# Kernel optimization log

Measured on AMD Instinct MI355X. Metric: run time of the kernel, lower is better.

Reference implementation:

```python
import jax, jax.numpy as jnp
import numpy as np

KERNEL_SIZE = 5
EPS = 1e-6


def setup_inputs() -> dict:
    key = jax.random.key(0)
    k1, k2 = jax.random.split(key)
    b, c, h, w = 16, 512, 64, 64
    hidden = 512
    input_dim = c + KERNEL_SIZE * KERNEL_SIZE  # 537
    x = jax.random.normal(k1, (b, c, h, w), dtype=jnp.float32)
    # 1x1 conv weight, stored as (out, in); kaiming-ish scale
    W = jax.random.normal(k2, (hidden, input_dim), dtype=jnp.float32) * (1.0 / np.sqrt(input_dim))
    bias = jnp.zeros((hidden,), dtype=jnp.float32)
    return {"x": x, "W": W, "bias": bias}


def spatial_descriptor(x, k):
    # x: (b,c,h,w) -> (b, k*k, h, w), local self-similarity (dot product) volume
    b, c, h, w = x.shape
    p = k // 2
    xp = jnp.pad(x, ((0, 0), (0, 0), (p, p), (p, p)))
    # small fixed loop over k*k offsets; each term is a fused multiply-reduce
    corrs = [
        jnp.sum(x * jax.lax.dynamic_slice(xp, (0, 0, di, dj), (b, c, h, w)), axis=1)
        for di in range(k)
        for dj in range(k)
    ]
    return jnp.stack(corrs, axis=1)  # (b, k*k, h, w)


def reference(x, W, bias):
    k = KERNEL_SIZE
    gs = spatial_descriptor(x, k)  # (b, k^2, h, w)
    # featureL2Norm over channel dim (note: eps added to sum-of-squares, then sqrt)
    norm = jnp.sqrt(jnp.sum(gs * gs, axis=1, keepdims=True) + EPS)
    gs = gs / norm
    feat = jnp.concatenate([x, gs], axis=1)  # (b, c+k^2, h, w)
    # 1x1 conv + ReLU
    out = jnp.einsum('bchw,oc->bohw', feat, W) + bias[None, :, None, None]
    return jax.nn.relu(out)
```

## Files before the change

kernel.cpp:

```cpp
#include <hip/hip_runtime.h>
#include <stdint.h>

#define C_IN 512
#define HW 4096
#define NPIX 65536
#define KPAD 544
#define KIN 537
#define HID 512

typedef __attribute__((ext_vector_type(8))) short bf16x8;
typedef __attribute__((ext_vector_type(4))) float f32x4;

__device__ __forceinline__ unsigned short f2bf(float f) {
  union { float f; uint32_t u; } v; v.f = f;
  uint32_t u = v.u;
  return (unsigned short)((u + 0x7fffu + ((u >> 16) & 1u)) >> 16);
}
__device__ __forceinline__ float bf2f(unsigned short h) {
  union { uint32_t u; float f; } v; v.u = ((uint32_t)h) << 16;
  return v.f;
}

__global__ void k_wconv(const float* __restrict__ W, unsigned short* __restrict__ Wb) {
  int idx = blockIdx.x * 256 + threadIdx.x;
  if (idx >= HID * KPAD) return;
  int o = idx / KPAD;
  int k = idx - o * KPAD;
  float v = (k < KIN) ? W[o * KIN + k] : 0.f;
  Wb[idx] = f2bf(v);
}

__global__ __launch_bounds__(256, 8) void k_xpose(const float* __restrict__ x,
                                                  unsigned short* __restrict__ featB) {
  __shared__ unsigned short sm[64][70];
  int g = blockIdx.x;
  int b = g >> 9, cg = (g >> 6) & 7, pt = g & 63;
  int c0 = cg * 64, p0 = pt * 64;
  int t = threadIdx.x, lane = t & 63, w = t >> 6;
  const float* xb = x + ((size_t)b * C_IN + c0) * HW + p0;
#pragma unroll
  for (int i = 0; i < 8; ++i) {
    int ch = w * 16 + i * 2;
    float a = xb[(size_t)ch * HW + lane];
    float bq = xb[(size_t)(ch + 1) * HW + lane];
    uint32_t pk = (uint32_t)f2bf(a) | ((uint32_t)f2bf(bq) << 16);
    *(uint32_t*)&sm[lane][ch] = pk;
  }
  __syncthreads();
#pragma unroll
  for (int i = 0; i < 2; ++i) {
    int px = (t >> 3) + i * 32, kg = t & 7;
    int n = b * 4096 + p0 + px;
    *(bf16x8*)(featB + (size_t)n * KPAD + c0 + kg * 8) = *(const bf16x8*)&sm[px][kg * 8];
  }
}

__device__ __forceinline__ int xelem(int sr, int sc, int kg) {
  return (sr * 20 + sc) * 64 + ((kg ^ (sc & 7)) * 8);
}

__global__ __launch_bounds__(256, 8) void k_corr(const unsigned short* __restrict__ featB,
                                                 unsigned short* __restrict__ part) {
  __shared__ unsigned short xt[8 * 20 * 64];
  int g = blockIdx.x;
  int bid = (g & 7) * 1024 + (g >> 3);
  int cs = bid & 7;
  int cg = (bid >> 3) & 3;
  int rg = (bid >> 5) & 15;
  int b  = bid >> 9;
  int t = threadIdx.x;
  int lane = t & 63;
  int w = t >> 6;
  int r0 = rg * 4, c0 = cg * 16;

  bf16x8 v[5];
  int la[5];
#pragma unroll
  for (int i = 0; i < 5; ++i) {
    int flat = t + i * 256;
    int kg = flat & 7, pxi = flat >> 3;
    int sc = pxi % 20, sr = pxi / 20;
    int ir = r0 - 2 + sr, ic = c0 - 2 + sc;
    la[i] = xelem(sr, sc, kg);
    if ((unsigned)ir < 64u && (unsigned)ic < 64u) {
      int n = b * 4096 + ir * 64 + ic;
      v[i] = *(const bf16x8*)(featB + (size_t)n * KPAD + cs * 64 + kg * 8);
    } else {
      v[i] = (bf16x8){0, 0, 0, 0, 0, 0, 0, 0};
    }
  }
#pragma unroll
  for (int i = 0; i < 5; ++i)
    *(bf16x8*)&xt[la[i]] = v[i];
  __syncthreads();

  int i15 = lane & 15;
  int tq = lane >> 4;
  int q = i15 - tq * 4;
  bool valid = (q >= 0) && (q < 4);

  bf16x8 afr[2];
#pragma unroll
  for (int ks = 0; ks < 2; ++ks)
    afr[ks] = *(const bf16x8*)&xt[xelem(w + 2, 2 + i15, ks * 4 + tq)];

  int nb = b * 4096 + (r0 + w) * 64 + c0;
#pragma unroll 1
  for (int di = 0; di < 5; ++di) {
    int sr = w + di;
    unsigned short* pbase = part + ((size_t)(cs * 25 + di * 5)) * NPIX + nb;
#pragma unroll
    for (int dj = 0; dj < 5; ++dj) {
      f32x4 acc = (f32x4){0.f, 0.f, 0.f, 0.f};
#pragma unroll
      for (int ks = 0; ks < 2; ++ks) {
        bf16x8 bfr = *(const bf16x8*)&xt[xelem(sr, dj + i15, ks * 4 + tq)];
        acc = __builtin_amdgcn_mfma_f32_16x16x32_bf16(afr[ks], bfr, acc, 0, 0, 0);
      }
      float val = (q == 0) ? acc[0]
                : (q == 1) ? acc[1]
                : (q == 2) ? acc[2] : acc[3];
      if (valid) pbase[(size_t)dj * NPIX + i15] = f2bf(val);
    }
  }
}

__global__ void k_norm(const unsigned short* __restrict__ part,
                       unsigned short* __restrict__ featB) {
  int n = blockIdx.x * 256 + threadIdx.x;
  float g[25];
  float ss = 0.f;
#pragma unroll
  for (int k = 0; k < 25; ++k) {
    float s = 0.f;
#pragma unroll
    for (int cs = 0; cs < 8; ++cs)
      s += bf2f(part[((size_t)cs * 25 + k) * NPIX + n]);
    g[k] = s;
    ss += s * s;
  }
  float inv = 1.0f / sqrtf(ss + 1e-6f);
  unsigned short buf[32];
#pragma unroll
  for (int k = 0; k < 25; ++k) buf[k] = f2bf(g[k] * inv);
#pragma unroll
  for (int k = 25; k < 32; ++k) buf[k] = 0;
#pragma unroll
  for (int j = 0; j < 4; ++j)
    *(bf16x8*)(featB + (size_t)n * KPAD + 512 + j * 8) = *(bf16x8*)&buf[j * 8];
}

typedef __attribute__((address_space(3))) unsigned int as3_uint;
typedef const __attribute__((address_space(1))) unsigned int as1_uint;

__device__ __forceinline__ void glds16(const void* g, void* l) {
  __builtin_amdgcn_global_load_lds((as1_uint*)g, (as3_uint*)l, 16, 0, 0);
}

__global__ __launch_bounds__(256) void k_gemm(const unsigned short* __restrict__ Wb,
                                              const unsigned short* __restrict__ featB,
                                              const float* __restrict__ bias,
                                              float* __restrict__ out) {
  __shared__ __attribute__((aligned(16))) unsigned short As[2][4096];
  __shared__ __attribute__((aligned(16))) unsigned short Bs[2][4096];
  int g = blockIdx.x;
  int bid = (g & 7) * 256 + (g >> 3);
  int mt = bid & 3;
  int nt = bid >> 2;
  int m0 = mt * 128;
  int n0 = nt * 128;
  int tid = threadIdx.x;
  int wave = tid >> 6;
  int lane = tid & 63;
  int wm = wave >> 1;
  int wn = wave & 1;
  int kg = lane >> 4;

  uint32_t aOff[4], bOff[4];
#pragma unroll
  for (int r = 0; r < 4; ++r) {
    int rr = wm * 64 + r * 16 + (lane & 15);
    aOff[r] = rr * 64 + ((kg ^ ((rr >> 1) & 3)) << 4);
  }
#pragma unroll
  for (int cb = 0; cb < 4; ++cb) {
    int rr = wn * 64 + cb * 16 + (lane & 15);
    bOff[cb] = rr * 64 + ((kg ^ ((rr >> 1) & 3)) << 4);
  }

  f32x4 acc[4][4];
#pragma unroll
  for (int r = 0; r < 4; ++r)
#pragma unroll
    for (int cb = 0; cb < 4; ++cb)
      acc[r][cb] = (f32x4){0.f, 0.f, 0.f, 0.f};

  auto STAGE = [&](int buf, int k0) {
#pragma unroll
    for (int qq = 0; qq < 2; ++qq) {
      int ci = wave * 2 + qq;
      int i = ci * 64 + lane;
      int rr = i >> 2;
      int slot = i & 3;
      int k8 = slot ^ ((rr >> 1) & 3);
      glds16(Wb + (size_t)(m0 + rr) * KPAD + k0 + k8 * 8, (char*)&As[buf][0] + ci * 1024);
      glds16(featB + (size_t)(n0 + rr) * KPAD + k0 + k8 * 8, (char*)&Bs[buf][0] + ci * 1024);
    }
  };

  STAGE(0, 0);
  __syncthreads();
  int cur = 0;
#pragma unroll 1
  for (int t = 0; t < 17; ++t) {
    if (t < 16) STAGE(cur ^ 1, (t + 1) * 32);
    const char* Ab = (const char*)&As[cur][0];
    const char* Bb = (const char*)&Bs[cur][0];
    bf16x8 af[4], bf[4];
#pragma unroll
    for (int r = 0; r < 4; ++r)
      af[r] = *(const bf16x8*)(Ab + aOff[r]);
#pragma unroll
    for (int cb = 0; cb < 4; ++cb)
      bf[cb] = *(const bf16x8*)(Bb + bOff[cb]);
#pragma unroll
    for (int cb = 0; cb < 4; ++cb)
#pragma unroll
      for (int r = 0; r < 4; ++r)
        acc[r][cb] = __builtin_amdgcn_mfma_f32_16x16x32_bf16(af[r], bf[cb], acc[r][cb], 0, 0, 0);
    __syncthreads();
    cur ^= 1;
  }

  int bb = n0 >> 12;
  int hwb = n0 & 4095;
  float* outb = out + (size_t)bb * (HID * HW) + hwb;
#pragma unroll
  for (int r = 0; r < 4; ++r) {
    int row0 = m0 + wm * 64 + r * 16 + (lane >> 4) * 4;
    float bv[4];
#pragma unroll
    for (int j = 0; j < 4; ++j) bv[j] = bias[row0 + j];
#pragma unroll
    for (int cb = 0; cb < 4; ++cb) {
      int col = wn * 64 + cb * 16 + (lane & 15);
#pragma unroll
      for (int j = 0; j < 4; ++j) {
        float v2 = acc[r][cb][j] + bv[j];
        v2 = fmaxf(v2, 0.f);
        outb[(size_t)(row0 + j) * HW + col] = v2;
      }
    }
  }
}

extern "C" void kernel_launch(void* const* d_in, const int* in_sizes, int n_in,
                              void* d_out, int out_size, void* d_ws, size_t ws_size,
                              hipStream_t stream) {
  const float* x = (const float*)d_in[0];
  const float* W = (const float*)d_in[1];
  const float* bias = (const float*)d_in[2];
  float* out = (float*)d_out;
  char* ws = (char*)d_ws;
  unsigned short* featB = (unsigned short*)ws;
  unsigned short* Wb = (unsigned short*)(ws + 71303168);
  unsigned short* part = (unsigned short*)(ws + 71860224);

  k_wconv<<<1088, 256, 0, stream>>>(W, Wb);
  k_xpose<<<8192, 256, 0, stream>>>(x, featB);
  k_corr<<<8192, 256, 0, stream>>>(featB, part);
  k_norm<<<256, 256, 0, stream>>>(part, featB);
  k_gemm<<<2048, 256, 0, stream>>>(Wb, featB, bias, out);
}
```

Measured before the change: 151.2 us.

## Fuse channel-split correlation and L2 normalization into one kernel

The correlation kernel now loops over all 8 channel slices inside each block and accumulates the 25 offsets in registers. It normalizes and writes the descriptor directly into the feature buffer, so the bf16 partial-sum buffer and the separate norm kernel are removed. This cuts a kernel launch and the global round-trip of the partials, and keeps the per-slice sums in fp32 rather than rounding them to bf16. The trade-off is 8x fewer blocks (1024), each running a serial loop with syncs and 25 extra accumulator registers, so there is less parallelism for hiding latency. The same buffer is passed as both the read-only and the written pointer, but the two touch disjoint columns.

```diff
diff --git a/kernel.cpp b/kernel.cpp
--- a/kernel.cpp
+++ b/kernel.cpp
@@ -15,10 +15,6 @@
   union { float f; uint32_t u; } v; v.f = f;
   uint32_t u = v.u;
   return (unsigned short)((u + 0x7fffu + ((u >> 16) & 1u)) >> 16);
-}
-__device__ __forceinline__ float bf2f(unsigned short h) {
-  union { uint32_t u; float f; } v; v.u = ((uint32_t)h) << 16;
-  return v.f;
 }
 
 __global__ void k_wconv(const float* __restrict__ W, unsigned short* __restrict__ Wb) {
@@ -59,95 +55,91 @@
   return (sr * 20 + sc) * 64 + ((kg ^ (sc & 7)) * 8);
 }
 
-__global__ __launch_bounds__(256, 8) void k_corr(const unsigned short* __restrict__ featB,
-                                                 unsigned short* __restrict__ part) {
+__global__ __launch_bounds__(256, 4) void k_corr(const unsigned short* __restrict__ featRO,
+                                                 unsigned short* __restrict__ featB) {
   __shared__ unsigned short xt[8 * 20 * 64];
   int g = blockIdx.x;
-  int bid = (g & 7) * 1024 + (g >> 3);
-  int cs = bid & 7;
-  int cg = (bid >> 3) & 3;
-  int rg = (bid >> 5) & 15;
-  int b  = bid >> 9;
+  int bid = (g & 7) * 128 + (g >> 3);
+  int cg = bid & 3;
+  int rg = (bid >> 2) & 15;
+  int b  = bid >> 6;
   int t = threadIdx.x;
   int lane = t & 63;
   int w = t >> 6;
   int r0 = rg * 4, c0 = cg * 16;
-
-  bf16x8 v[5];
-  int la[5];
-#pragma unroll
-  for (int i = 0; i < 5; ++i) {
-    int flat = t + i * 256;
-    int kg = flat & 7, pxi = flat >> 3;
-    int sc = pxi % 20, sr = pxi / 20;
-    int ir = r0 - 2 + sr, ic = c0 - 2 + sc;
-    la[i] = xelem(sr, sc, kg);
-    if ((unsigned)ir < 64u && (unsigned)ic < 64u) {
-      int n = b * 4096 + ir * 64 + ic;
-      v[i] = *(const bf16x8*)(featB + (size_t)n * KPAD + cs * 64 + kg * 8);
-    } else {
-      v[i] = (bf16x8){0, 0, 0, 0, 0, 0, 0, 0};
-    }
-  }
-#pragma unroll
-  for (int i = 0; i < 5; ++i)
-    *(bf16x8*)&xt[la[i]] = v[i];
-  __syncthreads();
-
   int i15 = lane & 15;
   int tq = lane >> 4;
   int q = i15 - tq * 4;
-  bool valid = (q >= 0) && (q < 4);
-
-  bf16x8 afr[2];
-#pragma unroll
-  for (int ks = 0; ks < 2; ++ks)
-    afr[ks] = *(const bf16x8*)&xt[xelem(w + 2, 2 + i15, ks * 4 + tq)];
-
-  int nb = b * 4096 + (r0 + w) * 64 + c0;
+  bool valid = (i15 >> 2) == tq;
+
+  float acc_s[25];
+#pragma unroll
+  for (int k = 0; k < 25; ++k) acc_s[k] = 0.f;
+
 #pragma unroll 1
-  for (int di = 0; di < 5; ++di) {
-    int sr = w + di;
-    unsigned short* pbase = part + ((size_t)(cs * 25 + di * 5)) * NPIX + nb;
-#pragma unroll
-    for (int dj = 0; dj < 5; ++dj) {
-      f32x4 acc = (f32x4){0.f, 0.f, 0.f, 0.f};
-#pragma unroll
-      for (int ks = 0; ks < 2; ++ks) {
-        bf16x8 bfr = *(const bf16x8*)&xt[xelem(sr, dj + i15, ks * 4 + tq)];
-        acc = __builtin_amdgcn_mfma_f32_16x16x32_bf16(afr[ks], bfr, acc, 0, 0, 0);
+  for (int cs = 0; cs < 8; ++cs) {
+    bf16x8 v[5];
+    int la[5];
+#pragma unroll
+    for (int i = 0; i < 5; ++i) {
+      int flat = t + i * 256;
+      int kg = flat & 7, pxi = flat >> 3;
+      int sc = pxi % 20, sr = pxi / 20;
+      int ir = r0 - 2 + sr, ic = c0 - 2 + sc;
+      la[i] = xelem(sr, sc, kg);
+      if ((unsigned)ir < 64u && (unsigned)ic < 64u) {
+        int n = b * 4096 + ir * 64 + ic;
+        v[i] = *(const bf16x8*)(featRO + (size_t)n * KPAD + cs * 64 + kg * 8);
+      } else {
+        v[i] = (bf16x8){0, 0, 0, 0, 0, 0, 0, 0};
       }
-      float val = (q == 0) ? acc[0]
-                : (q == 1) ? acc[1]
-                : (q == 2) ? acc[2] : acc[3];
-      if (valid) pbase[(size_t)dj * NPIX + i15] = f2bf(val);
-    }
-  }
-}
-
-__global__ void k_norm(const unsigned short* __restrict__ part,
-                       unsigned short* __restrict__ featB) {
-  int n = blockIdx.x * 256 + threadIdx.x;
-  float g[25];
-  float ss = 0.f;
-#pragma unroll
-  for (int k = 0; k < 25; ++k) {
-    float s = 0.f;
-#pragma unroll
-    for (int cs = 0; cs < 8; ++cs)
-      s += bf2f(part[((size_t)cs * 25 + k) * NPIX + n]);
-    g[k] = s;
-    ss += s * s;
-  }
-  float inv = 1.0f / sqrtf(ss + 1e-6f);
-  unsigned short buf[32];
-#pragma unroll
-  for (int k = 0; k < 25; ++k) buf[k] = f2bf(g[k] * inv);
-#pragma unroll
-  for (int k = 25; k < 32; ++k) buf[k] = 0;
-#pragma unroll
-  for (int j = 0; j < 4; ++j)
-    *(bf16x8*)(featB + (size_t)n * KPAD + 512 + j * 8) = *(bf16x8*)&buf[j * 8];
+    }
+#pragma unroll
+    for (int i = 0; i < 5; ++i)
+      *(bf16x8*)&xt[la[i]] = v[i];
+    __syncthreads();
+
+    bf16x8 afr[2];
+#pragma unroll
+    for (int ks = 0; ks < 2; ++ks)
+      afr[ks] = *(const bf16x8*)&xt[xelem(w + 2, 2 + i15, ks * 4 + tq)];
+
+#pragma unroll
+    for (int di = 0; di < 5; ++di) {
+      int sr = w + di;
+#pragma unroll
+      for (int dj = 0; dj < 5; ++dj) {
+        f32x4 acc = (f32x4){0.f, 0.f, 0.f, 0.f};
+#pragma unroll
+        for (int ks = 0; ks < 2; ++ks) {
+          bf16x8 bfr = *(const bf16x8*)&xt[xelem(sr, dj + i15, ks * 4 + tq)];
+          acc = __builtin_amdgcn_mfma_f32_16x16x32_bf16(afr[ks], bfr, acc, 0, 0, 0);
+        }
+        float val = (q == 0) ? acc[0]
+                  : (q == 1) ? acc[1]
+                  : (q == 2) ? acc[2] : acc[3];
+        acc_s[di * 5 + dj] += val;
+      }
+    }
+    __syncthreads();
+  }
+
+  if (valid) {
+    float ss = 0.f;
+#pragma unroll
+    for (int k = 0; k < 25; ++k) ss += acc_s[k] * acc_s[k];
+    float inv = 1.0f / sqrtf(ss + 1e-6f);
+    unsigned short buf[32];
+#pragma unroll
+    for (int k = 0; k < 25; ++k) buf[k] = f2bf(acc_s[k] * inv);
+#pragma unroll
+    for (int k = 25; k < 32; ++k) buf[k] = 0;
+    int n = b * 4096 + (r0 + w) * 64 + c0 + i15;
+    unsigned short* fb = featB + (size_t)n * KPAD + 512;
+#pragma unroll
+    for (int j = 0; j < 4; ++j)
+      *(bf16x8*)(fb + j * 8) = *(bf16x8*)&buf[j * 8];
+  }
 }
 
 typedef __attribute__((address_space(3))) unsigned int as3_uint;
@@ -264,11 +256,9 @@
   char* ws = (char*)d_ws;
   unsigned short* featB = (unsigned short*)ws;
   unsigned short* Wb = (unsigned short*)(ws + 71303168);
-  unsigned short* part = (unsigned short*)(ws + 71860224);
 
   k_wconv<<<1088, 256, 0, stream>>>(W, Wb);
   k_xpose<<<8192, 256, 0, stream>>>(x, featB);
-  k_corr<<<8192, 256, 0, stream>>>(featB, part);
-  k_norm<<<256, 256, 0, stream>>>(part, featB);
+  k_corr<<<1024, 256, 0, stream>>>(featB, featB);
   k_gemm<<<2048, 256, 0, stream>>>(Wb, featB, bias, out);
 }
```

Result: slower. 159.9 us (+5.7%).
